# Optimization experiments

Measured on AMD Instinct MI355X. Metric: run time of the kernel, lower is better.

The kernel has to match this reference:

```python
import jax, jax.numpy as jnp
import numpy as np

LN_EPS = 1e-5


def _mlp(x, W1, b1, W2, b2, g, beta):
    # build_mlp_d: Linear -> ReLU -> Linear -> LayerNorm (mlp_layers=2, lay_norm=True)
    h = jax.nn.relu(x @ W1 + b1)
    h = h @ W2 + b2
    mu = jnp.mean(h, axis=-1, keepdims=True)
    var = jnp.var(h, axis=-1, keepdims=True)
    return (h - mu) * jax.lax.rsqrt(var + LN_EPS) * g + beta


def setup_inputs() -> dict:
    E, N, L, EIF = 524288, 65536, 128, 3
    key = jax.random.key(0)
    ks = iter(jax.random.split(key, 48))
    def rn(shape, s=1.0):
        return jax.random.normal(next(ks), shape, dtype=jnp.float32) * s
    inp = {}
    inp["edge_index"] = jax.random.randint(next(ks), (2, E), 0, N)
    inp["edge_dx_"] = rn((E, 3))
    inp["edge_attr"] = rn((E, EIF))
    for nm in ["vector_a", "vector_b", "vector_c",
               "senders_v_t_", "senders_v_tm1_", "senders_w_t_", "senders_w_tm1_",
               "senders_a_t_", "senders_alpha_t_",
               "receivers_v_t_", "receivers_v_tm1_", "receivers_w_t_", "receivers_w_tm1_",
               "receivers_a_t_", "receivers_alpha_t_"]:
        inp[nm] = rn((E, 3))
    inp["node_latent"] = rn((N, L))
    def mlp_params(pfx, din):
        inp[pfx + "_W1"] = rn((din, L), 0.05)
        inp[pfx + "_b1"] = jnp.zeros((L,), jnp.float32)
        inp[pfx + "_W2"] = rn((L, L), 0.05)
        inp[pfx + "_b2"] = jnp.zeros((L,), jnp.float32)
        inp[pfx + "_g"] = jnp.ones((L,), jnp.float32)
        inp[pfx + "_beta"] = jnp.zeros((L,), jnp.float32)
    mlp_params("fe", 18)        # edge_feat_encoder
    mlp_params("ee", 1 + EIF)   # edge_encoder
    mlp_params("ie", 3 * L)     # interaction_encoder
    return inp


def reference(edge_index, edge_dx_, edge_attr, vector_a, vector_b, vector_c,
              senders_v_t_, senders_v_tm1_, senders_w_t_, senders_w_tm1_,
              senders_a_t_, senders_alpha_t_,
              receivers_v_t_, receivers_v_tm1_, receivers_w_t_, receivers_w_tm1_,
              receivers_a_t_, receivers_alpha_t_,
              node_latent,
              fe_W1, fe_b1, fe_W2, fe_b2, fe_g, fe_beta,
              ee_W1, ee_b1, ee_W2, ee_b2, ee_g, ee_beta,
              ie_W1, ie_b1, ie_W2, ie_b2, ie_g, ie_beta):
    senders, receivers = edge_index[0], edge_index[1]
    basis = jnp.stack([vector_a, vector_b, vector_c], axis=1)  # [E,3,3]
    # Fuse the 12 small bmm projections into two batched einsums.
    s_stack = jnp.stack([senders_v_t_, senders_v_tm1_, senders_w_t_, senders_w_tm1_,
                         senders_a_t_, senders_alpha_t_], axis=1)   # [E,6,3]
    r_stack = jnp.stack([receivers_v_t_, receivers_v_tm1_, receivers_w_t_, receivers_w_tm1_,
                         receivers_a_t_, receivers_alpha_t_], axis=1)
    s_proj = jnp.einsum('eij,ekj->eki', basis, s_stack)  # [E,6,3]
    r_proj = jnp.einsum('eij,ekj->eki', basis, r_stack)
    # signs: -v_t, -v_tm1, -w_t, +w_tm1, -a_t, +alpha_t (receivers side)
    r_sign = jnp.array([-1.0, -1.0, -1.0, 1.0, -1.0, 1.0], jnp.float32)[None, :, None]
    E = s_proj.shape[0]
    senders_features = s_proj.reshape(E, 18)
    receivers_features = (r_proj * r_sign).reshape(E, 18)
    edge_dx_norm = jnp.linalg.norm(edge_dx_, axis=1, keepdims=True)  # [E,1]
    edge_latent = _mlp(jnp.concatenate([edge_dx_norm, edge_attr], axis=1),
                       ee_W1, ee_b1, ee_W2, ee_b2, ee_g, ee_beta)
    senders_latent = _mlp(senders_features, fe_W1, fe_b1, fe_W2, fe_b2, fe_g, fe_beta)
    receivers_latent = _mlp(receivers_features, fe_W1, fe_b1, fe_W2, fe_b2, fe_g, fe_beta)
    node_sum = node_latent[senders] + node_latent[receivers]  # [E,L]
    msg_input = jnp.concatenate([senders_latent + receivers_latent, node_sum, edge_latent], axis=1)
    return _mlp(msg_input, ie_W1, ie_b1, ie_W2, ie_b2, ie_g, ie_beta)
```

## Files before the change

### kernel.cpp

```cpp
#include <hip/hip_runtime.h>

typedef __attribute__((ext_vector_type(4))) float fx4;
typedef __attribute__((ext_vector_type(8))) unsigned short u16x8;
typedef __attribute__((ext_vector_type(8))) __bf16 bf16x8;

static __device__ __forceinline__ unsigned short f2bf(float f) {
  unsigned int u = __builtin_bit_cast(unsigned int, f);
  u += 0x7fffu + ((u >> 16) & 1u);
  return (unsigned short)(u >> 16);
}
static __device__ __forceinline__ fx4 mfma16(u16x8 a, u16x8 b, fx4 c) {
  return __builtin_amdgcn_mfma_f32_16x16x32_bf16(
      __builtin_bit_cast(bf16x8, a), __builtin_bit_cast(bf16x8, b), c, 0, 0, 0);
}

static __device__ __forceinline__ int swz128(int row, int col) {
  return row * 128 + (col ^ ((row & 7) << 3));
}
static __device__ __forceinline__ int swz32(int row, int col) {
  return row * 32 + (col ^ (((row >> 1) & 3) << 3));
}

#define WT_FE1 0
#define WT_FE2 4096
#define WT_EE1 20480
#define WT_EE2 24576
#define WT_A   40960
#define WT_B   57344
#define WT_C   73728
#define WT_IE2 90112
#define WT_TOTAL 106496

__global__ void prep_weights(const float* __restrict__ feW1, const float* __restrict__ feW2,
                             const float* __restrict__ eeW1, const float* __restrict__ eeW2,
                             const float* __restrict__ ieW1, const float* __restrict__ ieW2,
                             unsigned short* __restrict__ wt) {
  int i = blockIdx.x * 256 + threadIdx.x;
  if (i >= WT_TOTAL) return;
  int base, n, k, kpad;
  float val;
  if (i < WT_FE2)      { base = WT_FE1; n = i >> 5; k = i & 31; kpad = 32;
                         val = (k < 18) ? feW1[k * 128 + n] : 0.f; }
  else if (i < WT_EE1) { base = WT_FE2; int j = i - WT_FE2; n = j >> 7; k = j & 127; kpad = 128;
                         val = feW2[k * 128 + n]; }
  else if (i < WT_EE2) { base = WT_EE1; int j = i - WT_EE1; n = j >> 5; k = j & 31; kpad = 32;
                         val = (k < 4) ? eeW1[k * 128 + n] : 0.f; }
  else if (i < WT_A)   { base = WT_EE2; int j = i - WT_EE2; n = j >> 7; k = j & 127; kpad = 128;
                         val = eeW2[k * 128 + n]; }
  else if (i < WT_B)   { base = WT_A;   int j = i - WT_A;   n = j >> 7; k = j & 127; kpad = 128;
                         val = ieW1[k * 128 + n]; }
  else if (i < WT_C)   { base = WT_B;   int j = i - WT_B;   n = j >> 7; k = j & 127; kpad = 128;
                         val = ieW1[(128 + k) * 128 + n]; }
  else if (i < WT_IE2) { base = WT_C;   int j = i - WT_C;   n = j >> 7; k = j & 127; kpad = 128;
                         val = ieW1[(256 + k) * 128 + n]; }
  else                 { base = WT_IE2; int j = i - WT_IE2; n = j >> 7; k = j & 127; kpad = 128;
                         val = ieW2[k * 128 + n]; }
  int dst = (kpad == 32) ? base + n * 32 + (k ^ (((n >> 1) & 3) << 3))
                         : base + n * 128 + (k ^ ((n & 7) << 3));
  wt[dst] = f2bf(val);
}

template<int KPAD, int KT>
static __device__ __forceinline__ void gemm_lds(const unsigned short* As,
                                                const unsigned short* Ws,
                                                fx4* acc, int l16, int lgr) {
#pragma unroll
  for (int kk = 0; kk < KT; kk++) {
    const int k0 = kk * 32 + lgr * 8;
    u16x8 af = *(const u16x8*)(As + ((KPAD == 32) ? swz32(l16, k0) : swz128(l16, k0)));
#pragma unroll
    for (int nt = 0; nt < 8; nt++) {
      const int n = nt * 16 + l16;
      u16x8 bf = *(const u16x8*)(Ws + ((KPAD == 32) ? swz32(n, k0) : swz128(n, k0)));
      acc[nt] = mfma16(af, bf, acc[nt]);
    }
  }
}

static __device__ __forceinline__ void relu_store(fx4* acc, const float* __restrict__ bias,
                                                  unsigned short* dst, int l16, int lgr) {
#pragma unroll
  for (int nt = 0; nt < 8; nt++) {
    const int col = nt * 16 + l16;
    const float b = bias[col];
#pragma unroll
    for (int r = 0; r < 4; r++) {
      float v = acc[nt][r] + b;
      dst[swz128(lgr * 4 + r, col)] = f2bf(v > 0.f ? v : 0.f);
    }
  }
}

static __device__ __forceinline__ void ln_rows(fx4* acc, const float* __restrict__ bias, int l16) {
  float sum[4] = {0, 0, 0, 0}, sq[4] = {0, 0, 0, 0};
#pragma unroll
  for (int nt = 0; nt < 8; nt++) {
    const float b = bias[nt * 16 + l16];
#pragma unroll
    for (int r = 0; r < 4; r++) {
      float v = acc[nt][r] + b; acc[nt][r] = v;
      sum[r] += v; sq[r] += v * v;
    }
  }
#pragma unroll
  for (int r = 0; r < 4; r++) {
    float s_ = sum[r], q_ = sq[r];
#pragma unroll
    for (int m = 1; m < 16; m <<= 1) { s_ += __shfl_xor(s_, m, 64); q_ += __shfl_xor(q_, m, 64); }
    const float mu = s_ * (1.f / 128.f);
    const float rs = rsqrtf(q_ * (1.f / 128.f) - mu * mu + 1e-5f);
#pragma unroll
    for (int nt = 0; nt < 8; nt++) acc[nt][r] = (acc[nt][r] - mu) * rs;
  }
}

struct ParamsFE {
  const float* basis[3];
  const float* sv[6]; const float* rv[6];
  const float* b1; const float* b2; const float* g; const float* be;
};
struct ParamsEE {
  const float* dx; const float* attr;
  const float* b1; const float* b2; const float* g; const float* be;
};

static __device__ __forceinline__ void fe_body(const ParamsFE& p, unsigned short* lds,
                                               const unsigned short* wt, unsigned short* msg,
                                               int bid, int nblocks, int ntiles) {
  const int tid = threadIdx.x;
  const int wave = tid >> 6, lane = tid & 63;
  const int l16 = lane & 15, lgr = lane >> 4;
#pragma unroll
  for (int i = tid * 8; i < 20480; i += 4096)
    *(u16x8*)(lds + i) = *(const u16x8*)(wt + WT_FE1 + i);
  const unsigned short* W1 = lds;
  const unsigned short* W2 = lds + 4096;
  unsigned short* h1 = lds + 20480 + wave * 2560;
  unsigned short* feat = h1 + 2048;
  __syncthreads();
#pragma unroll
  for (int j = 0; j < 4; j++) { int c = 18 + lgr * 4 + j; if (c < 32) feat[swz32(l16, c)] = 0; }
  const fx4 z4 = {0.f, 0.f, 0.f, 0.f};

  for (int t = bid; t < ntiles; t += nblocks) {
    const int e0 = t * 128 + wave * 16;
    const size_t e = (size_t)(e0 + l16);
    float bx[3][3];
#pragma unroll
    for (int i = 0; i < 3; i++) {
      const float* bp = p.basis[i] + 3 * e;
      bx[i][0] = bp[0]; bx[i][1] = bp[1]; bx[i][2] = bp[2];
    }
    fx4 latS[8];
#pragma unroll
    for (int side = 0; side < 2; side++) {
      const bool isR = (side == 1);
#pragma unroll
      for (int k = 0; k < 6; k++) {
        if ((k & 3) == lgr) {
          const float* vp = (isR ? p.rv[k] : p.sv[k]) + 3 * e;
          const float v0 = vp[0], v1 = vp[1], v2 = vp[2];
          const float sgn = (isR && k != 3 && k != 5) ? -1.f : 1.f;
#pragma unroll
          for (int i = 0; i < 3; i++) {
            float d = (bx[i][0] * v0 + bx[i][1] * v1 + bx[i][2] * v2) * sgn;
            feat[swz32(l16, k * 3 + i)] = f2bf(d);
          }
        }
      }
      fx4 acc[8];
#pragma unroll
      for (int b = 0; b < 8; b++) acc[b] = z4;
      gemm_lds<32, 1>(feat, W1, acc, l16, lgr);
      relu_store(acc, p.b1, h1, l16, lgr);
#pragma unroll
      for (int b = 0; b < 8; b++) acc[b] = z4;
      gemm_lds<128, 4>(h1, W2, acc, l16, lgr);
      ln_rows(acc, p.b2, l16);
      if (!isR) {
#pragma unroll
        for (int nt = 0; nt < 8; nt++) {
          const int col = nt * 16 + l16;
          const float gg = p.g[col], bb = p.be[col];
#pragma unroll
          for (int r = 0; r < 4; r++) latS[nt][r] = acc[nt][r] * gg + bb;
        }
      } else {
#pragma unroll
        for (int nt = 0; nt < 8; nt++) {
          const int col = nt * 16 + l16;
          const float gg = p.g[col], bb = p.be[col];
#pragma unroll
          for (int r = 0; r < 4; r++)
            msg[(size_t)(e0 + lgr * 4 + r) * 256 + col] =
                f2bf(latS[nt][r] + acc[nt][r] * gg + bb);
        }
      }
    }
  }
}

static __device__ __forceinline__ void ee_body(const ParamsEE& p, unsigned short* lds,
                                               const unsigned short* wt, unsigned short* msg,
                                               int bid, int nblocks, int ntiles) {
  const int tid = threadIdx.x;
  const int wave = tid >> 6, lane = tid & 63;
  const int l16 = lane & 15, lgr = lane >> 4;
#pragma unroll
  for (int i = tid * 8; i < 20480; i += 4096)
    *(u16x8*)(lds + i) = *(const u16x8*)(wt + WT_EE1 + i);
  const unsigned short* W1 = lds;
  const unsigned short* W2 = lds + 4096;
  unsigned short* h1 = lds + 20480 + wave * 2560;
  unsigned short* feat = h1 + 2048;
  __syncthreads();
#pragma unroll
  for (int j = 0; j < 7; j++) feat[swz32(l16, 4 + lgr * 7 + j)] = 0;
  const fx4 z4 = {0.f, 0.f, 0.f, 0.f};

  for (int t = bid; t < ntiles; t += nblocks) {
    const int e0 = t * 128 + wave * 16;
    const size_t e = (size_t)(e0 + l16);
    if (lgr == 0) {
      float d0 = p.dx[3 * e], d1 = p.dx[3 * e + 1], d2 = p.dx[3 * e + 2];
      feat[swz32(l16, 0)] = f2bf(sqrtf(d0 * d0 + d1 * d1 + d2 * d2));
    } else {
      feat[swz32(l16, lgr)] = f2bf(p.attr[3 * e + (lgr - 1)]);
    }
    fx4 acc[8];
#pragma unroll
    for (int b = 0; b < 8; b++) acc[b] = z4;
    gemm_lds<32, 1>(feat, W1, acc, l16, lgr);
    relu_store(acc, p.b1, h1, l16, lgr);
#pragma unroll
    for (int b = 0; b < 8; b++) acc[b] = z4;
    gemm_lds<128, 4>(h1, W2, acc, l16, lgr);
    ln_rows(acc, p.b2, l16);
#pragma unroll
    for (int nt = 0; nt < 8; nt++) {
      const int col = nt * 16 + l16;
      const float gg = p.g[col], bb = p.be[col];
#pragma unroll
      for (int r = 0; r < 4; r++)
        msg[(size_t)(e0 + lgr * 4 + r) * 256 + 128 + col] =
            f2bf(acc[nt][r] * gg + bb);
    }
  }
}

__global__ __launch_bounds__(512) void feee_kernel(ParamsFE pf, ParamsEE pe,
                                                   const unsigned short* wt,
                                                   unsigned short* msg,
                                                   int nfe, int ntiles) {
  extern __shared__ unsigned short lds[];
  if ((int)blockIdx.x < nfe)
    fe_body(pf, lds, wt, msg, blockIdx.x, nfe, ntiles);
  else
    ee_body(pe, lds, wt, msg, blockIdx.x - nfe, gridDim.x - nfe, ntiles);
}

struct ParamsIE {
  const int* eidx;
  const float* nl;
  const float* b1; const float* b2; const float* g; const float* be;
  const unsigned short* wt;
  const unsigned short* msg;
  float* out;
  int E; int nt16;
};

__global__ __launch_bounds__(768, 3) void ie_kernel(ParamsIE p) {
  extern __shared__ unsigned short dyn[];
  const int tid = threadIdx.x;
  const int wave = tid >> 6, lane = tid & 63;
  const int l16 = lane & 15, lgr = lane >> 4;
  for (int i = tid * 8; i < 49152; i += 6144)
    *(u16x8*)(dyn + i) = *(const u16x8*)(p.wt + WT_A + i);
  const unsigned short* WA = dyn;
  const unsigned short* WB = dyn + 16384;
  const unsigned short* WC = dyn + 32768;
  unsigned short* h1 = dyn + 49152 + wave * 2048;
  __syncthreads();
  const fx4 z4 = {0.f, 0.f, 0.f, 0.f};

  const int gw = blockIdx.x * 12 + wave;
  const int gstride = gridDim.x * 12;
  for (int t = gw; t < p.nt16; t += gstride) {
    const int e0 = t * 16;
    const size_t e = (size_t)(e0 + l16);
    const int sidx = p.eidx[e];
    const int ridx = p.eidx[(size_t)p.E + e];
    const unsigned short* mrow = p.msg + e * 256;
    const float* ns = p.nl + (size_t)sidx * 128;
    const float* nr = p.nl + (size_t)ridx * 128;
    fx4 acc[8];
#pragma unroll
    for (int b = 0; b < 8; b++) acc[b] = z4;
#pragma unroll
    for (int c = 0; c < 4; c++) {
      const int k0 = c * 32 + lgr * 8;
      fx4 a0 = *(const fx4*)(ns + k0), a1 = *(const fx4*)(ns + k0 + 4);
      fx4 b0 = *(const fx4*)(nr + k0), b1 = *(const fx4*)(nr + k0 + 4);
      u16x8 af;
#pragma unroll
      for (int j = 0; j < 4; j++) { af[j] = f2bf(a0[j] + b0[j]); af[4 + j] = f2bf(a1[j] + b1[j]); }
#pragma unroll
      for (int nt = 0; nt < 8; nt++) {
        u16x8 bf = *(const u16x8*)(WB + swz128(nt * 16 + l16, k0));
        acc[nt] = mfma16(af, bf, acc[nt]);
      }
    }
#pragma unroll
    for (int c = 0; c < 4; c++) {
      const int k0 = c * 32 + lgr * 8;
      u16x8 af = *(const u16x8*)(mrow + k0);
#pragma unroll
      for (int nt = 0; nt < 8; nt++) {
        u16x8 bf = *(const u16x8*)(WA + swz128(nt * 16 + l16, k0));
        acc[nt] = mfma16(af, bf, acc[nt]);
      }
    }
#pragma unroll
    for (int c = 0; c < 4; c++) {
      const int k0 = c * 32 + lgr * 8;
      u16x8 af = *(const u16x8*)(mrow + 128 + k0);
#pragma unroll
      for (int nt = 0; nt < 8; nt++) {
        u16x8 bf = *(const u16x8*)(WC + swz128(nt * 16 + l16, k0));
        acc[nt] = mfma16(af, bf, acc[nt]);
      }
    }
    relu_store(acc, p.b1, h1, l16, lgr);
#pragma unroll
    for (int b = 0; b < 8; b++) acc[b] = z4;
    gemm_lds<128, 4>(h1, p.wt + WT_IE2, acc, l16, lgr);
    ln_rows(acc, p.b2, l16);
#pragma unroll
    for (int nt = 0; nt < 8; nt++) {
      const int col = nt * 16 + l16;
      const float gg = p.g[col], bb = p.be[col];
#pragma unroll
      for (int r = 0; r < 4; r++)
        p.out[(size_t)(e0 + lgr * 4 + r) * 128 + col] = acc[nt][r] * gg + bb;
    }
  }
}

extern "C" void kernel_launch(void* const* d_in, const int* in_sizes, int n_in,
                              void* d_out, int out_size, void* d_ws, size_t ws_size,
                              hipStream_t stream) {
  (void)n_in; (void)out_size;
  const int E = in_sizes[1] / 3;
  unsigned short* wt = reinterpret_cast<unsigned short*>(d_ws);
  if (ws_size < (size_t)WT_TOTAL * sizeof(unsigned short)) return;

  prep_weights<<<(WT_TOTAL + 255) / 256, 256, 0, stream>>>(
      (const float*)d_in[19], (const float*)d_in[21],
      (const float*)d_in[25], (const float*)d_in[27],
      (const float*)d_in[31], (const float*)d_in[33], wt);

  unsigned short* msg = (unsigned short*)d_out;

  hipFuncSetAttribute((const void*)feee_kernel,
                      hipFuncAttributeMaxDynamicSharedMemorySize, 81920);
  hipFuncSetAttribute((const void*)ie_kernel,
                      hipFuncAttributeMaxDynamicSharedMemorySize, 147456);

  ParamsFE pf;
  for (int i = 0; i < 3; i++) pf.basis[i] = (const float*)d_in[3 + i];
  for (int k = 0; k < 6; k++) { pf.sv[k] = (const float*)d_in[6 + k]; pf.rv[k] = (const float*)d_in[12 + k]; }
  pf.b1 = (const float*)d_in[20]; pf.b2 = (const float*)d_in[22];
  pf.g  = (const float*)d_in[23]; pf.be = (const float*)d_in[24];

  ParamsEE pe;
  pe.dx = (const float*)d_in[1]; pe.attr = (const float*)d_in[2];
  pe.b1 = (const float*)d_in[26]; pe.b2 = (const float*)d_in[28];
  pe.g  = (const float*)d_in[29]; pe.be = (const float*)d_in[30];

  feee_kernel<<<1024, 512, 81920, stream>>>(pf, pe, wt, msg, 512, E / 128);

  ParamsIE pi;
  pi.eidx = (const int*)d_in[0];
  pi.nl = (const float*)d_in[18];
  pi.b1 = (const float*)d_in[32]; pi.b2 = (const float*)d_in[34];
  pi.g  = (const float*)d_in[35]; pi.be = (const float*)d_in[36];
  pi.wt = wt; pi.msg = msg; pi.out = (float*)d_out;
  pi.E = E; pi.nt16 = E / 16;
  ie_kernel<<<256, 768, 147456, stream>>>(pi);
}
```

Measured before the change: 639.0 us.

## Batch sender/receiver FE MLPs together, shrink blocks, retile IE kernel

The FE path now builds sender and receiver features together in one 32-row tile and runs both through shared weight-fragment loads, so each W1/W2 LDS read feeds two MFMAs. Block sizes drop from 512 to 256 threads for FE/EE, with a larger grid and 64-edge tiles. The IE kernel moves to 512-thread blocks with 128-edge per-block tiles, 8 waves per block and less dynamic LDS. The intent is more weight reuse from LDS and a different occupancy balance, at the cost of more accumulator registers per wave.

```diff
diff --git a/kernel.cpp b/kernel.cpp
--- a/kernel.cpp
+++ b/kernel.cpp
@@ -131,19 +131,22 @@
   const int wave = tid >> 6, lane = tid & 63;
   const int l16 = lane & 15, lgr = lane >> 4;
 #pragma unroll
-  for (int i = tid * 8; i < 20480; i += 4096)
+  for (int i = tid * 8; i < 20480; i += 2048)
     *(u16x8*)(lds + i) = *(const u16x8*)(wt + WT_FE1 + i);
   const unsigned short* W1 = lds;
   const unsigned short* W2 = lds + 4096;
-  unsigned short* h1 = lds + 20480 + wave * 2560;
-  unsigned short* feat = h1 + 2048;
+  unsigned short* h1 = lds + 20480 + wave * 5120;
+  unsigned short* feat = h1 + 4096;
   __syncthreads();
 #pragma unroll
-  for (int j = 0; j < 4; j++) { int c = 18 + lgr * 4 + j; if (c < 32) feat[swz32(l16, c)] = 0; }
+  for (int j = 0; j < 4; j++) {
+    int c = 18 + lgr * 4 + j;
+    if (c < 32) { feat[swz32(l16, c)] = 0; feat[swz32(16 + l16, c)] = 0; }
+  }
   const fx4 z4 = {0.f, 0.f, 0.f, 0.f};
 
   for (int t = bid; t < ntiles; t += nblocks) {
-    const int e0 = t * 128 + wave * 16;
+    const int e0 = t * 64 + wave * 16;
     const size_t e = (size_t)(e0 + l16);
     float bx[3][3];
 #pragma unroll
@@ -151,51 +154,63 @@
       const float* bp = p.basis[i] + 3 * e;
       bx[i][0] = bp[0]; bx[i][1] = bp[1]; bx[i][2] = bp[2];
     }
-    fx4 latS[8];
-#pragma unroll
-    for (int side = 0; side < 2; side++) {
-      const bool isR = (side == 1);
-#pragma unroll
-      for (int k = 0; k < 6; k++) {
-        if ((k & 3) == lgr) {
-          const float* vp = (isR ? p.rv[k] : p.sv[k]) + 3 * e;
-          const float v0 = vp[0], v1 = vp[1], v2 = vp[2];
-          const float sgn = (isR && k != 3 && k != 5) ? -1.f : 1.f;
-#pragma unroll
-          for (int i = 0; i < 3; i++) {
-            float d = (bx[i][0] * v0 + bx[i][1] * v1 + bx[i][2] * v2) * sgn;
-            feat[swz32(l16, k * 3 + i)] = f2bf(d);
-          }
+#pragma unroll
+    for (int k = 0; k < 6; k++) {
+      if ((k & 3) == lgr) {
+        const float* vs = p.sv[k] + 3 * e;
+        const float* vr = p.rv[k] + 3 * e;
+        const float s0 = vs[0], s1 = vs[1], s2 = vs[2];
+        const float r0 = vr[0], r1 = vr[1], r2 = vr[2];
+        const float sgn = (k != 3 && k != 5) ? -1.f : 1.f;
+#pragma unroll
+        for (int i = 0; i < 3; i++) {
+          feat[swz32(l16, k * 3 + i)] =
+              f2bf(bx[i][0] * s0 + bx[i][1] * s1 + bx[i][2] * s2);
+          feat[swz32(16 + l16, k * 3 + i)] =
+              f2bf((bx[i][0] * r0 + bx[i][1] * r1 + bx[i][2] * r2) * sgn);
         }
       }
-      fx4 acc[8];
-#pragma unroll
-      for (int b = 0; b < 8; b++) acc[b] = z4;
-      gemm_lds<32, 1>(feat, W1, acc, l16, lgr);
-      relu_store(acc, p.b1, h1, l16, lgr);
-#pragma unroll
-      for (int b = 0; b < 8; b++) acc[b] = z4;
-      gemm_lds<128, 4>(h1, W2, acc, l16, lgr);
-      ln_rows(acc, p.b2, l16);
-      if (!isR) {
-#pragma unroll
-        for (int nt = 0; nt < 8; nt++) {
-          const int col = nt * 16 + l16;
-          const float gg = p.g[col], bb = p.be[col];
-#pragma unroll
-          for (int r = 0; r < 4; r++) latS[nt][r] = acc[nt][r] * gg + bb;
-        }
-      } else {
-#pragma unroll
-        for (int nt = 0; nt < 8; nt++) {
-          const int col = nt * 16 + l16;
-          const float gg = p.g[col], bb = p.be[col];
-#pragma unroll
-          for (int r = 0; r < 4; r++)
-            msg[(size_t)(e0 + lgr * 4 + r) * 256 + col] =
-                f2bf(latS[nt][r] + acc[nt][r] * gg + bb);
-        }
-      }
+    }
+    fx4 accA[8], accB[8];
+#pragma unroll
+    for (int b = 0; b < 8; b++) { accA[b] = z4; accB[b] = z4; }
+    {
+      const int k0 = lgr * 8;
+      u16x8 afA = *(const u16x8*)(feat + swz32(l16, k0));
+      u16x8 afB = *(const u16x8*)(feat + swz32(16 + l16, k0));
+#pragma unroll
+      for (int nt = 0; nt < 8; nt++) {
+        u16x8 bf = *(const u16x8*)(W1 + swz32(nt * 16 + l16, k0));
+        accA[nt] = mfma16(afA, bf, accA[nt]);
+        accB[nt] = mfma16(afB, bf, accB[nt]);
+      }
+    }
+    relu_store(accA, p.b1, h1, l16, lgr);
+    relu_store(accB, p.b1, h1 + 2048, l16, lgr);
+#pragma unroll
+    for (int b = 0; b < 8; b++) { accA[b] = z4; accB[b] = z4; }
+#pragma unroll
+    for (int c = 0; c < 4; c++) {
+      const int k0 = c * 32 + lgr * 8;
+      u16x8 afA = *(const u16x8*)(h1 + swz128(l16, k0));
+      u16x8 afB = *(const u16x8*)(h1 + 2048 + swz128(l16, k0));
+#pragma unroll
+      for (int nt = 0; nt < 8; nt++) {
+        u16x8 bf = *(const u16x8*)(W2 + swz128(nt * 16 + l16, k0));
+        accA[nt] = mfma16(afA, bf, accA[nt]);
+        accB[nt] = mfma16(afB, bf, accB[nt]);
+      }
+    }
+    ln_rows(accA, p.b2, l16);
+    ln_rows(accB, p.b2, l16);
+#pragma unroll
+    for (int nt = 0; nt < 8; nt++) {
+      const int col = nt * 16 + l16;
+      const float gg = p.g[col], bb = p.be[col];
+#pragma unroll
+      for (int r = 0; r < 4; r++)
+        msg[(size_t)(e0 + lgr * 4 + r) * 256 + col] =
+            f2bf(accA[nt][r] * gg + bb + accB[nt][r] * gg + bb);
     }
   }
 }
@@ -207,7 +222,7 @@
   const int wave = tid >> 6, lane = tid & 63;
   const int l16 = lane & 15, lgr = lane >> 4;
 #pragma unroll
-  for (int i = tid * 8; i < 20480; i += 4096)
+  for (int i = tid * 8; i < 20480; i += 2048)
     *(u16x8*)(lds + i) = *(const u16x8*)(wt + WT_EE1 + i);
   const unsigned short* W1 = lds;
   const unsigned short* W2 = lds + 4096;
@@ -219,7 +234,7 @@
   const fx4 z4 = {0.f, 0.f, 0.f, 0.f};
 
   for (int t = bid; t < ntiles; t += nblocks) {
-    const int e0 = t * 128 + wave * 16;
+    const int e0 = t * 64 + wave * 16;
     const size_t e = (size_t)(e0 + l16);
     if (lgr == 0) {
       float d0 = p.dx[3 * e], d1 = p.dx[3 * e + 1], d2 = p.dx[3 * e + 2];
@@ -248,7 +263,7 @@
   }
 }
 
-__global__ __launch_bounds__(512) void feee_kernel(ParamsFE pf, ParamsEE pe,
+__global__ __launch_bounds__(256) void feee_kernel(ParamsFE pf, ParamsEE pe,
                                                    const unsigned short* wt,
                                                    unsigned short* msg,
                                                    int nfe, int ntiles) {
@@ -266,15 +281,16 @@
   const unsigned short* wt;
   const unsigned short* msg;
   float* out;
-  int E; int nt16;
+  int E; int ntiles;
 };
 
-__global__ __launch_bounds__(768, 3) void ie_kernel(ParamsIE p) {
+__global__ __launch_bounds__(512) void ie_kernel(ParamsIE p) {
   extern __shared__ unsigned short dyn[];
   const int tid = threadIdx.x;
   const int wave = tid >> 6, lane = tid & 63;
   const int l16 = lane & 15, lgr = lane >> 4;
-  for (int i = tid * 8; i < 49152; i += 6144)
+#pragma unroll
+  for (int i = tid * 8; i < 49152; i += 4096)
     *(u16x8*)(dyn + i) = *(const u16x8*)(p.wt + WT_A + i);
   const unsigned short* WA = dyn;
   const unsigned short* WB = dyn + 16384;
@@ -283,10 +299,8 @@
   __syncthreads();
   const fx4 z4 = {0.f, 0.f, 0.f, 0.f};
 
-  const int gw = blockIdx.x * 12 + wave;
-  const int gstride = gridDim.x * 12;
-  for (int t = gw; t < p.nt16; t += gstride) {
-    const int e0 = t * 16;
+  for (int t = blockIdx.x; t < p.ntiles; t += gridDim.x) {
+    const int e0 = t * 128 + wave * 16;
     const size_t e = (size_t)(e0 + l16);
     const int sidx = p.eidx[e];
     const int ridx = p.eidx[(size_t)p.E + e];
@@ -364,7 +378,7 @@
   hipFuncSetAttribute((const void*)feee_kernel,
                       hipFuncAttributeMaxDynamicSharedMemorySize, 81920);
   hipFuncSetAttribute((const void*)ie_kernel,
-                      hipFuncAttributeMaxDynamicSharedMemorySize, 147456);
+                      hipFuncAttributeMaxDynamicSharedMemorySize, 131072);
 
   ParamsFE pf;
   for (int i = 0; i < 3; i++) pf.basis[i] = (const float*)d_in[3 + i];
@@ -377,7 +391,7 @@
   pe.b1 = (const float*)d_in[26]; pe.b2 = (const float*)d_in[28];
   pe.g  = (const float*)d_in[29]; pe.be = (const float*)d_in[30];
 
-  feee_kernel<<<1024, 512, 81920, stream>>>(pf, pe, wt, msg, 512, E / 128);
+  feee_kernel<<<1536, 256, 81920, stream>>>(pf, pe, wt, msg, 1024, E / 64);
 
   ParamsIE pi;
   pi.eidx = (const int*)d_in[0];
@@ -385,6 +399,6 @@
   pi.b1 = (const float*)d_in[32]; pi.b2 = (const float*)d_in[34];
   pi.g  = (const float*)d_in[35]; pi.be = (const float*)d_in[36];
   pi.wt = wt; pi.msg = msg; pi.out = (float*)d_out;
-  pi.E = E; pi.nt16 = E / 16;
-  ie_kernel<<<256, 768, 147456, stream>>>(pi);
-}
+  pi.E = E; pi.ntiles = E / 128;
+  ie_kernel<<<256, 512, 131072, stream>>>(pi);
+}
```

Measured after the change: 523.8 us. 1.22x faster.
